# Performance work log

Hardware: AMD Instinct MI355X
Metric: run time of the kernel (lower is better)

The kernel has to match this reference:

```python
import jax, jax.numpy as jnp
from jax import lax
import numpy as np

B, H, W, D_MODEL = 2, 64, 64, 192
D_INNER, D_STATE, DT_RANK = 384, 16, 12
L = H * W
LN_EPS = 1e-5


def setup_inputs() -> dict:
    ks = jax.random.split(jax.random.key(0), 12)
    rng = np.random.default_rng(0)
    perm = rng.permutation(L).astype(np.int32)

    def p(i, shape, scale=0.02):
        return jax.random.normal(ks[i], shape, dtype=jnp.float32) * scale

    return {
        "x": jax.random.normal(ks[0], (B, H, W, D_MODEL), dtype=jnp.float32),
        "condition": jax.random.normal(ks[1], (B, H, W, D_MODEL), dtype=jnp.float32),
        "W_in": p(2, (2 * D_INNER, D_MODEL)),
        "W_con": p(3, (D_INNER, D_MODEL)),
        "conv_w": p(4, (D_INNER, 1, 3, 3)),
        "conv_b": jnp.zeros((D_INNER,), jnp.float32),
        "con_conv_w": p(5, (D_INNER, 1, 3, 3)),
        "con_conv_b": jnp.zeros((D_INNER,), jnp.float32),
        "x_proj_w": p(6, (DT_RANK + 2 * D_STATE, D_INNER)),
        "dt_proj_w": p(7, (D_INNER, DT_RANK)),
        "dt_proj_b": p(8, (D_INNER,), 0.1),
        "A_logs": jnp.tile(jnp.log(jnp.arange(1, D_STATE + 1, dtype=jnp.float32))[None, :], (D_INNER, 1)),
        "Ds": jnp.ones((D_INNER,), jnp.float32),
        "ln_w": jnp.ones((D_INNER,), jnp.float32),
        "ln_b": jnp.zeros((D_INNER,), jnp.float32),
        "W_out": p(9, (D_MODEL, D_INNER)),
        "scan_path": jnp.asarray(perm),
        "rev_scan_path": jnp.asarray(np.argsort(perm).astype(np.int32)),
    }


def _dwconv(x, w, b):
    # depthwise 3x3 conv, SAME padding; x: [B, C, H, W], w: [C, 1, 3, 3]
    y = lax.conv_general_dilated(x, w, (1, 1), "SAME",
                                 dimension_numbers=("NCHW", "OIHW", "NCHW"),
                                 feature_group_count=x.shape[1])
    return y + b[None, :, None, None]


def _selective_scan(u, delta, A, Bs, Cs, D):
    # u, delta: [B, D, L]; A: [D, N]; Bs, Cs: [B, N, L]; D: [D]
    dA = jnp.exp(jnp.einsum("bdl,dn->lbdn", delta, A))          # [L, B, D, N]
    dBu = jnp.einsum("bdl,bnl,bdl->lbdn", delta, Bs, u)          # [L, B, D, N]
    Ct = jnp.transpose(Cs, (2, 0, 1))                             # [L, B, N]
    h0 = jnp.zeros(dA.shape[1:], dA.dtype)

    def step(h, inp):
        a, b, c = inp
        h = a * h + b
        return h, jnp.einsum("bdn,bn->bd", h, c)

    _, ys = lax.scan(step, h0, (dA, dBu, Ct))                     # ys: [L, B, D]
    y = jnp.transpose(ys, (1, 2, 0))                              # [B, D, L]
    return y + u * D[None, :, None]


def _forward(x, condition, W_in, W_con, conv_w, conv_b, con_conv_w, con_conv_b,
             x_proj_w, dt_proj_w, dt_proj_b, A_logs, Ds, ln_w, ln_b, W_out,
             scan_path, rev_scan_path):
    b, h, w, _ = x.shape
    l = h * w
    xz = x @ W_in.T                                               # [B, H, W, 2*Din]
    xa, z = jnp.split(xz, 2, axis=-1)
    z = jax.nn.silu(z)
    c = condition @ W_con.T
    xa = jax.nn.silu(_dwconv(jnp.transpose(xa, (0, 3, 1, 2)), conv_w, conv_b))
    c = jax.nn.silu(_dwconv(jnp.transpose(c, (0, 3, 1, 2)), con_conv_w, con_conv_b))
    d = xa.shape[1]
    xs = xa.reshape(b, d, l)[:, :, scan_path]                     # forward_permutation, K=1
    cs = c.reshape(b, d, l)[:, :, scan_path]
    x_dbl = jnp.einsum("bdl,cd->bcl", xs + cs, x_proj_w)          # [B, R+2N, L]
    r, n = dt_proj_w.shape[1], A_logs.shape[1]
    dts = jnp.einsum("brl,dr->bdl", x_dbl[:, :r], dt_proj_w)
    Bs = x_dbl[:, r:r + n]
    Cs = x_dbl[:, r + n:]
    A = -jnp.exp(A_logs)
    delta = jax.nn.softplus(dts + dt_proj_b[None, :, None])       # delta_softplus=True
    y = _selective_scan(xs, delta, A, Bs, Cs, Ds)                 # [B, D, L]
    y = y[:, :, rev_scan_path]                                    # backward_permutation
    y = jnp.transpose(y, (0, 2, 1))                               # [B, L, D]
    mu = jnp.mean(y, axis=-1, keepdims=True)
    var = jnp.var(y, axis=-1, keepdims=True)
    y = (y - mu) * lax.rsqrt(var + LN_EPS) * ln_w + ln_b          # out_norm
    y = y.reshape(b, h, w, d) * z
    return y @ W_out.T                                            # out_proj (no bias)


def reference(x, condition, W_in, W_con, conv_w, conv_b, con_conv_w, con_conv_b,
              x_proj_w, dt_proj_w, dt_proj_b, A_logs, Ds, ln_w, ln_b, W_out,
              scan_path, rev_scan_path):
    return _forward(x, condition, W_in, W_con, conv_w, conv_b, con_conv_w,
                    con_conv_b, x_proj_w, dt_proj_w, dt_proj_b, A_logs, Ds,
                    ln_w, ln_b, W_out, scan_path, rev_scan_path)
```

## Files before the change

### kernel.cpp

```cpp
#include <hip/hip_runtime.h>
#include <math.h>

#define BB 2
#define HH 64
#define WW 64
#define DM 192
#define DI 384
#define NS 16
#define DTR 12
#define LL 4096
#define ROWS (BB*LL)
#define NCHUNK 64
#define LCHUNK 64
#define NCOMB 448

typedef __attribute__((ext_vector_type(8))) short bf16x8;
typedef __attribute__((ext_vector_type(4))) float f32x4;

__device__ __forceinline__ float silu_f(float v) {
    return v / (1.0f + __expf(-v));
}

__device__ __forceinline__ unsigned short f2bf(float f) {
    union { float f; unsigned int u; } c; c.f = f;
    unsigned int u = c.u;
    u += 0x7fffu + ((u >> 16) & 1u);
    return (unsigned short)(u >> 16);
}
__device__ __forceinline__ float bf2f(unsigned short h) {
    union { unsigned int u; float f; } c; c.u = ((unsigned int)h) << 16;
    return c.f;
}

__device__ __forceinline__ bf16x8 f2bf8(float4 a, float4 b) {
    bf16x8 r;
    r[0] = (short)f2bf(a.x); r[1] = (short)f2bf(a.y);
    r[2] = (short)f2bf(a.z); r[3] = (short)f2bf(a.w);
    r[4] = (short)f2bf(b.x); r[5] = (short)f2bf(b.y);
    r[6] = (short)f2bf(b.z); r[7] = (short)f2bf(b.w);
    return r;
}

__global__ __launch_bounds__(256) void prep_weights(
    const float* __restrict__ w_in, const float* __restrict__ w_con,
    const float* __restrict__ w_out,
    const float* __restrict__ x_proj_w, const float* __restrict__ dt_w,
    unsigned short* __restrict__ w_in_bf, unsigned short* __restrict__ w_con_bf,
    unsigned short* __restrict__ w_out_bf, unsigned short* __restrict__ wc)
{
    int idx = blockIdx.x * 256 + threadIdx.x;
    if (idx < 73728) {
        const float4* src; ushort4* dst; int off;
        if (idx < 36864)      { src = (const float4*)w_in;  dst = (ushort4*)w_in_bf;  off = idx; }
        else if (idx < 55296) { src = (const float4*)w_con; dst = (ushort4*)w_con_bf; off = idx - 36864; }
        else                  { src = (const float4*)w_out; dst = (ushort4*)w_out_bf; off = idx - 55296; }
        float4 v = src[off];
        ushort4 o;
        o.x = f2bf(v.x); o.y = f2bf(v.y); o.z = f2bf(v.z); o.w = f2bf(v.w);
        dst[off] = o;
    } else {
        int e = idx - 73728;
        if (e >= NCOMB * DI) return;
        int row = e / DI, k = e - row * DI;
        float v = 0.f;
        if (row < 384) {
            const float* dw = dt_w + row * DTR;
            #pragma unroll
            for (int r = 0; r < DTR; ++r) v += dw[r] * x_proj_w[r * DI + k];
        } else if (row < 416) {
            v = x_proj_w[(12 + (row - 384)) * DI + k];
        }
        wc[e] = f2bf(v);
    }
}

__device__ __forceinline__ void gemm_epilogue(
    int mode, int row, int col, int N, float v,
    const float* __restrict__ bias,
    float* __restrict__ out0, void* __restrict__ out1)
{
    if (mode == 0) {
        if (col < 384) out0[(size_t)row * 384 + col] = v;
        else ((unsigned short*)out1)[(size_t)row * 384 + (col - 384)] = f2bf(silu_f(v));
    } else if (mode == 1) {
        out0[(size_t)row * N + col] = v;
    } else {
        if (col < 384) {
            float a = v + bias[col];
            out0[(size_t)row * 384 + col] = (a > 20.f) ? a : log1pf(__expf(a));
        } else if (col < 416) {
            int idx = col - 384;
            int pos = (idx < 16) ? ((idx & 7) * 4 + (idx >> 3))
                                 : (((idx - 16) & 7) * 4 + 2 + ((idx - 16) >> 3));
            ((float*)out1)[(size_t)row * 32 + pos] = v;
        }
    }
}

__global__ __launch_bounds__(256) void gemm_bf16(
    const unsigned short* __restrict__ A, const unsigned short* __restrict__ W,
    const float* __restrict__ bias,
    float* __restrict__ out0, void* __restrict__ out1,
    int M, int N, int K, int mode)
{
    __shared__ __align__(16) unsigned short sA[64 * 40];
    __shared__ __align__(16) unsigned short sB[64 * 40];
    const int bm = blockIdx.x * 64;
    const int bn = blockIdx.y * 64;
    const int tid  = threadIdx.x;
    const int wave = tid >> 6;
    const int lane = tid & 63;
    const int quad = lane >> 4;
    const int l16  = lane & 15;
    const int lrow = tid >> 2;
    const int lkof = (tid & 3) * 8;

    f32x4 acc[4];
    #pragma unroll
    for (int t = 0; t < 4; ++t) acc[t] = (f32x4)(0.f);

    const int arow = (wave * 16 + l16) * 40 + quad * 8;

    for (int k0 = 0; k0 < K; k0 += 32) {
        *(bf16x8*)&sA[lrow * 40 + lkof] =
            *(const bf16x8*)&A[(size_t)(bm + lrow) * K + k0 + lkof];
        *(bf16x8*)&sB[lrow * 40 + lkof] =
            *(const bf16x8*)&W[(size_t)(bn + lrow) * K + k0 + lkof];
        __syncthreads();
        bf16x8 a = *(bf16x8*)&sA[arow];
        #pragma unroll
        for (int t = 0; t < 4; ++t) {
            bf16x8 b = *(bf16x8*)&sB[(t * 16 + l16) * 40 + quad * 8];
            acc[t] = __builtin_amdgcn_mfma_f32_16x16x32_bf16(a, b, acc[t], 0, 0, 0);
        }
        __syncthreads();
    }

    #pragma unroll
    for (int t = 0; t < 4; ++t) {
        int col = bn + t * 16 + l16;
        #pragma unroll
        for (int r = 0; r < 4; ++r) {
            int row = bm + wave * 16 + quad * 4 + r;
            gemm_epilogue(mode, row, col, N, acc[t][r], bias, out0, out1);
        }
    }
}

__global__ __launch_bounds__(256) void gemm_dual(
    const float* __restrict__ x, const float* __restrict__ cond,
    const unsigned short* __restrict__ w_in_bf,
    const unsigned short* __restrict__ w_con_bf,
    float* __restrict__ xa_pre, unsigned short* __restrict__ z_bf,
    float* __restrict__ c_pre)
{
    const int zz = blockIdx.z;
    if (zz == 1 && blockIdx.y >= 6) return;
    const float* A = zz ? cond : x;
    const unsigned short* W = zz ? w_con_bf : w_in_bf;
    float* out0 = zz ? c_pre : xa_pre;
    const int mode = zz ? 1 : 0;
    const int N = zz ? 384 : 768;

    __shared__ __align__(16) unsigned short sA[64 * 40];
    __shared__ __align__(16) unsigned short sB[64 * 40];
    const int bm = blockIdx.x * 64;
    const int bn = blockIdx.y * 64;
    const int tid  = threadIdx.x;
    const int wave = tid >> 6;
    const int lane = tid & 63;
    const int quad = lane >> 4;
    const int l16  = lane & 15;
    const int lrow = tid >> 2;
    const int lkof = (tid & 3) * 8;

    f32x4 acc[4];
    #pragma unroll
    for (int t = 0; t < 4; ++t) acc[t] = (f32x4)(0.f);

    const int arow = (wave * 16 + l16) * 40 + quad * 8;

    for (int k0 = 0; k0 < DM; k0 += 32) {
        const float* ap = &A[(size_t)(bm + lrow) * DM + k0 + lkof];
        float4 a0 = *(const float4*)ap;
        float4 a1 = *(const float4*)(ap + 4);
        *(bf16x8*)&sA[lrow * 40 + lkof] = f2bf8(a0, a1);
        *(bf16x8*)&sB[lrow * 40 + lkof] =
            *(const bf16x8*)&W[(size_t)(bn + lrow) * DM + k0 + lkof];
        __syncthreads();
        bf16x8 a = *(bf16x8*)&sA[arow];
        #pragma unroll
        for (int t = 0; t < 4; ++t) {
            bf16x8 b = *(bf16x8*)&sB[(t * 16 + l16) * 40 + quad * 8];
            acc[t] = __builtin_amdgcn_mfma_f32_16x16x32_bf16(a, b, acc[t], 0, 0, 0);
        }
        __syncthreads();
    }

    #pragma unroll
    for (int t = 0; t < 4; ++t) {
        int col = bn + t * 16 + l16;
        #pragma unroll
        for (int r = 0; r < 4; ++r) {
            int row = bm + wave * 16 + quad * 4 + r;
            gemm_epilogue(mode, row, col, N, acc[t][r], nullptr, out0, (void*)z_bf);
        }
    }
}

__global__ __launch_bounds__(256) void dwconv2_scatter(
    const float* __restrict__ xin, const float* __restrict__ cin,
    const float* __restrict__ wx, const float* __restrict__ bx,
    const float* __restrict__ wc, const float* __restrict__ bc,
    const int* __restrict__ rev_scan_path,
    float* __restrict__ xs_buf, unsigned short* __restrict__ s_bf)
{
    const int tile = blockIdx.x;
    const int c0   = blockIdx.y * 32;
    const int b    = blockIdx.z;
    const int h0 = (tile >> 3) * 8, w0 = (tile & 7) * 8;
    __shared__ float smx[10 * 10 * 32];
    __shared__ float smc[10 * 10 * 32];
    __shared__ int   jtile[64];

    for (int idx = threadIdx.x; idx < 3200; idx += 256) {
        int pix = idx >> 5, ch = idx & 31;
        int py = pix / 10, px = pix - py * 10;
        int gh = h0 + py - 1, gw = w0 + px - 1;
        float vx = 0.f, vc = 0.f;
        if (gh >= 0 && gh < 64 && gw >= 0 && gw < 64) {
            size_t g = ((size_t)(b * LL + gh * 64 + gw)) * DI + c0 + ch;
            vx = xin[g]; vc = cin[g];
        }
        smx[idx] = vx; smc[idx] = vc;
    }
    if (threadIdx.x < 64) {
        int l = (h0 + (threadIdx.x >> 3)) * 64 + (w0 + (threadIdx.x & 7));
        jtile[threadIdx.x] = rev_scan_path[l];
    }
    __syncthreads();

    const int ch = threadIdx.x & 31;
    const int pq = threadIdx.x >> 5;
    float wrx[9], wrc[9];
    #pragma unroll
    for (int k = 0; k < 9; ++k) {
        wrx[k] = wx[(c0 + ch) * 9 + k];
        wrc[k] = wc[(c0 + ch) * 9 + k];
    }
    const float bvx = bx[c0 + ch];
    const float bvc = bc[c0 + ch];

    #pragma unroll
    for (int i = 0; i < 8; ++i) {
        int p  = pq * 8 + i;
        int ph = p >> 3, pw = p & 7;
        float ax = bvx, ac = bvc;
        #pragma unroll
        for (int ki = 0; ki < 3; ++ki)
            #pragma unroll
            for (int kj = 0; kj < 3; ++kj) {
                int si = ((ph + ki) * 10 + (pw + kj)) * 32 + ch;
                ax += wrx[ki * 3 + kj] * smx[si];
                ac += wrc[ki * 3 + kj] * smc[si];
            }
        float xv = silu_f(ax);
        float sv = xv + silu_f(ac);
        size_t o = ((size_t)(b * LL + jtile[p])) * DI + c0 + ch;
        xs_buf[o] = xv;
        s_bf[o]   = f2bf(sv);
    }
}

__global__ __launch_bounds__(256) void scan_chunkA(
    const float* __restrict__ xs, const float* __restrict__ delta,
    const float* __restrict__ btct, const float* __restrict__ A_logs,
    float* __restrict__ chunkA, float* __restrict__ chunkB)
{
    const int c = blockIdx.x;
    const int g = blockIdx.y;
    const int b = blockIdx.z;
    const int t = threadIdx.x;
    const int grp = t >> 3, p = t & 7;
    const int d = g * 32 + grp;
    const float Av0 = -__expf(A_logs[d * NS + p]);
    const float Av1 = -__expf(A_logs[d * NS + p + 8]);
    const int j0 = c * LCHUNK;

    const float*  dl = delta + ((size_t)b * LL + j0) * DI + d;
    const float*  ul = xs    + ((size_t)b * LL + j0) * DI + d;
    const float2* bl = (const float2*)btct + ((size_t)b * LL + j0) * 16 + p * 2;

    float h0 = 0.f, h1 = 0.f, Sd = 0.f;
    float dv[4], uv[4]; float2 bv[4];
    #pragma unroll
    for (int q = 0; q < 4; ++q) {
        dv[q] = dl[(size_t)q * DI]; uv[q] = ul[(size_t)q * DI]; bv[q] = bl[(size_t)q * 16];
    }
    for (int j = 0; j < LCHUNK; j += 4) {
        float nd[4], nu[4]; float2 nb[4];
        if (j + 4 < LCHUNK) {
            #pragma unroll
            for (int q = 0; q < 4; ++q) {
                int jj = j + 4 + q;
                nd[q] = dl[(size_t)jj * DI]; nu[q] = ul[(size_t)jj * DI]; nb[q] = bl[(size_t)jj * 16];
            }
        }
        #pragma unroll
        for (int q = 0; q < 4; ++q) {
            float e0 = __expf(dv[q] * Av0);
            float e1 = __expf(dv[q] * Av1);
            float du = dv[q] * uv[q];
            h0 = e0 * h0 + bv[q].x * du;
            h1 = e1 * h1 + bv[q].y * du;
            Sd += dv[q];
        }
        #pragma unroll
        for (int q = 0; q < 4; ++q) { dv[q]=nd[q]; uv[q]=nu[q]; bv[q]=nb[q]; }
    }
    size_t idx = (((size_t)b * DI + d) * 8 + p) * NCHUNK + c;
    ((float2*)chunkA)[idx] = make_float2(__expf(Sd * Av0), __expf(Sd * Av1));
    ((float2*)chunkB)[idx] = make_float2(h0, h1);
}

__global__ __launch_bounds__(256) void scan_combine(
    const float* __restrict__ chunkA, const float* __restrict__ chunkB,
    float* __restrict__ hstart)
{
    const int gid = blockIdx.x * 256 + threadIdx.x;
    const float2* A2 = (const float2*)chunkA + (size_t)gid * NCHUNK;
    const float2* B2 = (const float2*)chunkB + (size_t)gid * NCHUNK;
    float2*       H2 = (float2*)hstart       + (size_t)gid * NCHUNK;
    float h0 = 0.f, h1 = 0.f;
    for (int c = 0; c < NCHUNK; ++c) {
        float2 a = A2[c], bv = B2[c];
        H2[c] = make_float2(h0, h1);
        h0 = a.x * h0 + bv.x;
        h1 = a.y * h1 + bv.y;
    }
}

__global__ __launch_bounds__(256) void scan_chunkC(
    const float* __restrict__ xs, const float* __restrict__ delta,
    const float* __restrict__ btct,
    const float* __restrict__ A_logs, const float* __restrict__ Ds,
    const float* __restrict__ hstart,
    float* __restrict__ yt)
{
    const int c = blockIdx.x;
    const int g = blockIdx.y;
    const int b = blockIdx.z;
    const int t = threadIdx.x;
    const int grp = t >> 3, p = t & 7;
    const int d = g * 32 + grp;
    const float Av0 = -__expf(A_logs[d * NS + p]);
    const float Av1 = -__expf(A_logs[d * NS + p + 8]);
    const float Dv = Ds[d];
    const int j0 = c * LCHUNK;

    const float*  dl  = delta + ((size_t)b * LL + j0) * DI + d;
    const float*  ul  = xs    + ((size_t)b * LL + j0) * DI + d;
    const float4* bcl = (const float4*)btct + ((size_t)b * LL + j0) * 8 + p;
    float* yl = yt + ((size_t)b * LL + j0) * DI + d;

    float2 h = ((const float2*)hstart)[(((size_t)b * DI + d) * 8 + p) * NCHUNK + c];
    float h0 = h.x, h1 = h.y;

    float dv[4], uv[4]; float4 bc[4];
    #pragma unroll
    for (int q = 0; q < 4; ++q) {
        dv[q] = dl[(size_t)q * DI]; uv[q] = ul[(size_t)q * DI]; bc[q] = bcl[(size_t)q * 8];
    }
    for (int j = 0; j < LCHUNK; j += 4) {
        float nd[4], nu[4]; float4 nbc[4];
        if (j + 4 < LCHUNK) {
            #pragma unroll
            for (int q = 0; q < 4; ++q) {
                int jj = j + 4 + q;
                nd[q] = dl[(size_t)jj * DI]; nu[q] = ul[(size_t)jj * DI]; nbc[q] = bcl[(size_t)jj * 8];
            }
        }
        #pragma unroll
        for (int q = 0; q < 4; ++q) {
            float e0 = __expf(dv[q] * Av0);
            float e1 = __expf(dv[q] * Av1);
            float du = dv[q] * uv[q];
            h0 = e0 * h0 + bc[q].x * du;
            h1 = e1 * h1 + bc[q].y * du;
            float acc = h0 * bc[q].z + h1 * bc[q].w;
            acc += __shfl_xor(acc, 4, 8);
            acc += __shfl_xor(acc, 2, 8);
            acc += __shfl_xor(acc, 1, 8);
            if (p == 0) yl[(size_t)(j + q) * DI] = acc + uv[q] * Dv;
        }
        #pragma unroll
        for (int q = 0; q < 4; ++q) { dv[q]=nd[q]; uv[q]=nu[q]; bc[q]=nbc[q]; }
    }
}

__global__ __launch_bounds__(128) void ln_mul(
    const float* __restrict__ yt, const unsigned short* __restrict__ z,
    const int* __restrict__ scan_path,
    const float* __restrict__ ln_w, const float* __restrict__ ln_b,
    unsigned short* __restrict__ yn)
{
    const int j = blockIdx.x;
    const int b = blockIdx.y;
    const int l = scan_path[j];
    const int t = threadIdx.x;
    const float* row = yt + ((size_t)(b * LL + j)) * DI;
    float v0 = row[t], v1 = row[t + 128], v2 = row[t + 256];
    float s  = v0 + v1 + v2;
    float s2 = v0*v0 + v1*v1 + v2*v2;
    #pragma unroll
    for (int off = 32; off > 0; off >>= 1) {
        s  += __shfl_down(s, off);
        s2 += __shfl_down(s2, off);
    }
    __shared__ float red[4];
    if ((t & 63) == 0) { red[(t >> 6) * 2] = s; red[(t >> 6) * 2 + 1] = s2; }
    __syncthreads();
    float S  = red[0] + red[2];
    float S2 = red[1] + red[3];
    float mu  = S * (1.0f / DI);
    float var = S2 * (1.0f / DI) - mu * mu;
    float inv = rsqrtf(var + 1e-5f);

    const unsigned short* zr = z + ((size_t)(b * LL + l)) * DI;
    unsigned short* o = yn + ((size_t)(b * LL + l)) * DI;
    o[t]       = f2bf(((v0 - mu) * inv * ln_w[t]       + ln_b[t])       * bf2f(zr[t]));
    o[t + 128] = f2bf(((v1 - mu) * inv * ln_w[t + 128] + ln_b[t + 128]) * bf2f(zr[t + 128]));
    o[t + 256] = f2bf(((v2 - mu) * inv * ln_w[t + 256] + ln_b[t + 256]) * bf2f(zr[t + 256]));
}

extern "C" void kernel_launch(void* const* d_in, const int* in_sizes, int n_in,
                              void* d_out, int out_size, void* d_ws, size_t ws_size,
                              hipStream_t stream) {
    const float* x          = (const float*)d_in[0];
    const float* cond       = (const float*)d_in[1];
    const float* W_in       = (const float*)d_in[2];
    const float* W_con      = (const float*)d_in[3];
    const float* conv_w     = (const float*)d_in[4];
    const float* conv_b     = (const float*)d_in[5];
    const float* con_conv_w = (const float*)d_in[6];
    const float* con_conv_b = (const float*)d_in[7];
    const float* x_proj_w   = (const float*)d_in[8];
    const float* dt_proj_w  = (const float*)d_in[9];
    const float* dt_proj_b  = (const float*)d_in[10];
    const float* A_logs     = (const float*)d_in[11];
    const float* Ds         = (const float*)d_in[12];
    const float* ln_w       = (const float*)d_in[13];
    const float* ln_b       = (const float*)d_in[14];
    const float* W_out      = (const float*)d_in[15];
    const int*   scan_path  = (const int*)d_in[16];
    const int*   rev_path   = (const int*)d_in[17];

    float* ws = (float*)d_ws;
    const size_t S  = (size_t)BB * LL * DI;
    const size_t SC = (size_t)NCHUNK * BB * DI * NS;
    float* xa_pre  = ws + 0 * S;
    float* zslab   = ws + 1 * S;
    float* c_pre   = ws + 2 * S;
    float* xs_buf  = ws + 3 * S;
    float* dl_buf  = ws + 4 * S;
    float* btct    = ws + 5 * S;
    float* chunkA  = btct + (size_t)BB * LL * 32;
    float* chunkB  = chunkA + SC;
    float* hstart  = chunkB + SC;
    float* bfpool  = hstart + SC;

    unsigned short* z_bf     = (unsigned short*)zslab;
    unsigned short* s_bf     = (unsigned short*)bfpool;
    unsigned short* w_in_bf  = s_bf + (size_t)ROWS * DI;
    unsigned short* w_con_bf = w_in_bf + 768 * DM;
    unsigned short* w_out_bf = w_con_bf + 384 * DM;
    unsigned short* wcomb_bf = w_out_bf + 192 * DI;
    unsigned short* yn_bf    = (unsigned short*)c_pre;
    float* yt = xa_pre;

    prep_weights<<<(73728 + NCOMB * DI + 255) / 256, 256, 0, stream>>>(
        W_in, W_con, W_out, x_proj_w, dt_proj_w,
        w_in_bf, w_con_bf, w_out_bf, wcomb_bf);

    gemm_dual<<<dim3(ROWS / 64, 12, 2), 256, 0, stream>>>(
        x, cond, w_in_bf, w_con_bf, xa_pre, z_bf, c_pre);
    dwconv2_scatter<<<dim3(64, 12, BB), 256, 0, stream>>>(
        xa_pre, c_pre, conv_w, conv_b, con_conv_w, con_conv_b,
        rev_path, xs_buf, s_bf);
    gemm_bf16<<<dim3(ROWS / 64, NCOMB / 64), 256, 0, stream>>>(
        s_bf, wcomb_bf, dt_proj_b, dl_buf, (void*)btct, ROWS, NCOMB, DI, 2);
    scan_chunkA<<<dim3(NCHUNK, DI / 32, BB), 256, 0, stream>>>(
        xs_buf, dl_buf, btct, A_logs, chunkA, chunkB);
    scan_combine<<<(BB * DI * 8) / 256, 256, 0, stream>>>(chunkA, chunkB, hstart);
    scan_chunkC<<<dim3(NCHUNK, DI / 32, BB), 256, 0, stream>>>(
        xs_buf, dl_buf, btct, A_logs, Ds, hstart, yt);
    ln_mul<<<dim3(LL, BB), 128, 0, stream>>>(yt, z_bf, scan_path, ln_w, ln_b, yn_bf);
    gemm_bf16<<<dim3(ROWS / 64, 192 / 64), 256, 0, stream>>>(
        yn_bf, w_out_bf, nullptr, (float*)d_out, nullptr, ROWS, DM, DI, 1);
}
```

Measured before the change: 231.8 us.

## Fuse chunked scan into single-pass kernel with decoupled lookback

Replaces the three scan kernels (chunk-local reduction, serial combine, chunk replay) with one kernel. Each block takes a dynamic ticket for its chunk, publishes its local decay and state with a release flag, then walks back over predecessor chunks with acquire spins, stopping early once the accumulated decay underflows. This removes two kernel launches and the hstart/chunk buffer round trip, at the cost of spin-waiting, serial lookback latency for later chunks and an approximation that truncates negligible contributions.

After: 454.6 us. 1.96x slower.

```diff
diff --git a/kernel.cpp b/kernel.cpp
--- a/kernel.cpp
+++ b/kernel.cpp
@@ -13,6 +13,7 @@
 #define NCHUNK 64
 #define LCHUNK 64
 #define NCOMB 448
+#define NSEQ (12*BB)
 
 typedef __attribute__((ext_vector_type(8))) short bf16x8;
 typedef __attribute__((ext_vector_type(4))) float f32x4;
@@ -46,7 +47,8 @@
     const float* __restrict__ w_out,
     const float* __restrict__ x_proj_w, const float* __restrict__ dt_w,
     unsigned short* __restrict__ w_in_bf, unsigned short* __restrict__ w_con_bf,
-    unsigned short* __restrict__ w_out_bf, unsigned short* __restrict__ wc)
+    unsigned short* __restrict__ w_out_bf, unsigned short* __restrict__ wc,
+    int* __restrict__ flags_tickets)
 {
     int idx = blockIdx.x * 256 + threadIdx.x;
     if (idx < 73728) {
@@ -58,9 +60,8 @@
         ushort4 o;
         o.x = f2bf(v.x); o.y = f2bf(v.y); o.z = f2bf(v.z); o.w = f2bf(v.w);
         dst[off] = o;
-    } else {
+    } else if (idx < 73728 + NCOMB * DI) {
         int e = idx - 73728;
-        if (e >= NCOMB * DI) return;
         int row = e / DI, k = e - row * DI;
         float v = 0.f;
         if (row < 384) {
@@ -71,6 +72,9 @@
             v = x_proj_w[(12 + (row - 384)) * DI + k];
         }
         wc[e] = f2bf(v);
+    } else {
+        int e = idx - (73728 + NCOMB * DI);
+        if (e < NSEQ * NCHUNK + NSEQ) flags_tickets[e] = 0;
     }
 }
 
@@ -272,84 +276,20 @@
     }
 }
 
-__global__ __launch_bounds__(256) void scan_chunkA(
-    const float* __restrict__ xs, const float* __restrict__ delta,
-    const float* __restrict__ btct, const float* __restrict__ A_logs,
-    float* __restrict__ chunkA, float* __restrict__ chunkB)
-{
-    const int c = blockIdx.x;
-    const int g = blockIdx.y;
-    const int b = blockIdx.z;
-    const int t = threadIdx.x;
-    const int grp = t >> 3, p = t & 7;
-    const int d = g * 32 + grp;
-    const float Av0 = -__expf(A_logs[d * NS + p]);
-    const float Av1 = -__expf(A_logs[d * NS + p + 8]);
-    const int j0 = c * LCHUNK;
-
-    const float*  dl = delta + ((size_t)b * LL + j0) * DI + d;
-    const float*  ul = xs    + ((size_t)b * LL + j0) * DI + d;
-    const float2* bl = (const float2*)btct + ((size_t)b * LL + j0) * 16 + p * 2;
-
-    float h0 = 0.f, h1 = 0.f, Sd = 0.f;
-    float dv[4], uv[4]; float2 bv[4];
-    #pragma unroll
-    for (int q = 0; q < 4; ++q) {
-        dv[q] = dl[(size_t)q * DI]; uv[q] = ul[(size_t)q * DI]; bv[q] = bl[(size_t)q * 16];
-    }
-    for (int j = 0; j < LCHUNK; j += 4) {
-        float nd[4], nu[4]; float2 nb[4];
-        if (j + 4 < LCHUNK) {
-            #pragma unroll
-            for (int q = 0; q < 4; ++q) {
-                int jj = j + 4 + q;
-                nd[q] = dl[(size_t)jj * DI]; nu[q] = ul[(size_t)jj * DI]; nb[q] = bl[(size_t)jj * 16];
-            }
-        }
-        #pragma unroll
-        for (int q = 0; q < 4; ++q) {
-            float e0 = __expf(dv[q] * Av0);
-            float e1 = __expf(dv[q] * Av1);
-            float du = dv[q] * uv[q];
-            h0 = e0 * h0 + bv[q].x * du;
-            h1 = e1 * h1 + bv[q].y * du;
-            Sd += dv[q];
-        }
-        #pragma unroll
-        for (int q = 0; q < 4; ++q) { dv[q]=nd[q]; uv[q]=nu[q]; bv[q]=nb[q]; }
-    }
-    size_t idx = (((size_t)b * DI + d) * 8 + p) * NCHUNK + c;
-    ((float2*)chunkA)[idx] = make_float2(__expf(Sd * Av0), __expf(Sd * Av1));
-    ((float2*)chunkB)[idx] = make_float2(h0, h1);
-}
-
-__global__ __launch_bounds__(256) void scan_combine(
-    const float* __restrict__ chunkA, const float* __restrict__ chunkB,
-    float* __restrict__ hstart)
-{
-    const int gid = blockIdx.x * 256 + threadIdx.x;
-    const float2* A2 = (const float2*)chunkA + (size_t)gid * NCHUNK;
-    const float2* B2 = (const float2*)chunkB + (size_t)gid * NCHUNK;
-    float2*       H2 = (float2*)hstart       + (size_t)gid * NCHUNK;
-    float h0 = 0.f, h1 = 0.f;
-    for (int c = 0; c < NCHUNK; ++c) {
-        float2 a = A2[c], bv = B2[c];
-        H2[c] = make_float2(h0, h1);
-        h0 = a.x * h0 + bv.x;
-        h1 = a.y * h1 + bv.y;
-    }
-}
-
-__global__ __launch_bounds__(256) void scan_chunkC(
+__global__ __launch_bounds__(256) void scan_single(
     const float* __restrict__ xs, const float* __restrict__ delta,
     const float* __restrict__ btct,
     const float* __restrict__ A_logs, const float* __restrict__ Ds,
-    const float* __restrict__ hstart,
-    float* __restrict__ yt)
-{
-    const int c = blockIdx.x;
+    float4* __restrict__ Loc, int* __restrict__ flags,
+    int* __restrict__ tickets, float* __restrict__ yt)
+{
     const int g = blockIdx.y;
     const int b = blockIdx.z;
+    const int seq = g * BB + b;
+    __shared__ int sc;
+    if (threadIdx.x == 0) sc = atomicAdd(&tickets[seq], 1);
+    __syncthreads();
+    const int c = sc;
     const int t = threadIdx.x;
     const int grp = t >> 3, p = t & 7;
     const int d = g * 32 + grp;
@@ -360,41 +300,96 @@
 
     const float*  dl  = delta + ((size_t)b * LL + j0) * DI + d;
     const float*  ul  = xs    + ((size_t)b * LL + j0) * DI + d;
+    const float2* bl  = (const float2*)btct + ((size_t)b * LL + j0) * 16 + p * 2;
     const float4* bcl = (const float4*)btct + ((size_t)b * LL + j0) * 8 + p;
     float* yl = yt + ((size_t)b * LL + j0) * DI + d;
 
-    float2 h = ((const float2*)hstart)[(((size_t)b * DI + d) * 8 + p) * NCHUNK + c];
-    float h0 = h.x, h1 = h.y;
-
-    float dv[4], uv[4]; float4 bc[4];
-    #pragma unroll
-    for (int q = 0; q < 4; ++q) {
-        dv[q] = dl[(size_t)q * DI]; uv[q] = ul[(size_t)q * DI]; bc[q] = bcl[(size_t)q * 8];
-    }
-    for (int j = 0; j < LCHUNK; j += 4) {
-        float nd[4], nu[4]; float4 nbc[4];
-        if (j + 4 < LCHUNK) {
+    float h0 = 0.f, h1 = 0.f, Sd = 0.f;
+    {
+        float dv[4], uv[4]; float2 bv[4];
+        #pragma unroll
+        for (int q = 0; q < 4; ++q) {
+            dv[q] = dl[(size_t)q * DI]; uv[q] = ul[(size_t)q * DI]; bv[q] = bl[(size_t)q * 16];
+        }
+        for (int j = 0; j < LCHUNK; j += 4) {
+            float nd[4], nu[4]; float2 nb[4];
+            if (j + 4 < LCHUNK) {
+                #pragma unroll
+                for (int q = 0; q < 4; ++q) {
+                    int jj = j + 4 + q;
+                    nd[q] = dl[(size_t)jj * DI]; nu[q] = ul[(size_t)jj * DI]; nb[q] = bl[(size_t)jj * 16];
+                }
+            }
             #pragma unroll
             for (int q = 0; q < 4; ++q) {
-                int jj = j + 4 + q;
-                nd[q] = dl[(size_t)jj * DI]; nu[q] = ul[(size_t)jj * DI]; nbc[q] = bcl[(size_t)jj * 8];
+                float e0 = __expf(dv[q] * Av0);
+                float e1 = __expf(dv[q] * Av1);
+                float du = dv[q] * uv[q];
+                h0 = e0 * h0 + bv[q].x * du;
+                h1 = e1 * h1 + bv[q].y * du;
+                Sd += dv[q];
             }
-        }
+            #pragma unroll
+            for (int q = 0; q < 4; ++q) { dv[q]=nd[q]; uv[q]=nu[q]; bv[q]=nb[q]; }
+        }
+    }
+    const float A0 = __expf(Sd * Av0), A1 = __expf(Sd * Av1);
+
+    const size_t lbase = ((size_t)seq * NCHUNK + c) * 256;
+    Loc[lbase + t] = make_float4(A0, A1, h0, h1);
+    __threadfence();
+    __syncthreads();
+    if (t == 0)
+        __hip_atomic_store(&flags[seq * NCHUNK + c], 1,
+                           __ATOMIC_RELEASE, __HIP_MEMORY_SCOPE_AGENT);
+
+    float hs0 = 0.f, hs1 = 0.f, P0 = 1.f, P1 = 1.f;
+    for (int i = c - 1; i >= 0; --i) {
+        if (t == 0) {
+            while (__hip_atomic_load(&flags[seq * NCHUNK + i],
+                                     __ATOMIC_ACQUIRE, __HIP_MEMORY_SCOPE_AGENT) == 0)
+                __builtin_amdgcn_s_sleep(8);
+        }
+        __syncthreads();
+        float4 L = Loc[((size_t)seq * NCHUNK + i) * 256 + t];
+        hs0 += P0 * L.z;  hs1 += P1 * L.w;
+        P0  *= L.x;       P1  *= L.y;
+        int dead = (fabsf(P0) < 1e-35f) && (fabsf(P1) < 1e-35f);
+        if (__syncthreads_and(dead)) break;
+    }
+
+    h0 = hs0; h1 = hs1;
+    {
+        float dv[4], uv[4]; float4 bc[4];
         #pragma unroll
         for (int q = 0; q < 4; ++q) {
-            float e0 = __expf(dv[q] * Av0);
-            float e1 = __expf(dv[q] * Av1);
-            float du = dv[q] * uv[q];
-            h0 = e0 * h0 + bc[q].x * du;
-            h1 = e1 * h1 + bc[q].y * du;
-            float acc = h0 * bc[q].z + h1 * bc[q].w;
-            acc += __shfl_xor(acc, 4, 8);
-            acc += __shfl_xor(acc, 2, 8);
-            acc += __shfl_xor(acc, 1, 8);
-            if (p == 0) yl[(size_t)(j + q) * DI] = acc + uv[q] * Dv;
-        }
-        #pragma unroll
-        for (int q = 0; q < 4; ++q) { dv[q]=nd[q]; uv[q]=nu[q]; bc[q]=nbc[q]; }
+            dv[q] = dl[(size_t)q * DI]; uv[q] = ul[(size_t)q * DI]; bc[q] = bcl[(size_t)q * 8];
+        }
+        for (int j = 0; j < LCHUNK; j += 4) {
+            float nd[4], nu[4]; float4 nbc[4];
+            if (j + 4 < LCHUNK) {
+                #pragma unroll
+                for (int q = 0; q < 4; ++q) {
+                    int jj = j + 4 + q;
+                    nd[q] = dl[(size_t)jj * DI]; nu[q] = ul[(size_t)jj * DI]; nbc[q] = bcl[(size_t)jj * 8];
+                }
+            }
+            #pragma unroll
+            for (int q = 0; q < 4; ++q) {
+                float e0 = __expf(dv[q] * Av0);
+                float e1 = __expf(dv[q] * Av1);
+                float du = dv[q] * uv[q];
+                h0 = e0 * h0 + bc[q].x * du;
+                h1 = e1 * h1 + bc[q].y * du;
+                float acc = h0 * bc[q].z + h1 * bc[q].w;
+                acc += __shfl_xor(acc, 4, 8);
+                acc += __shfl_xor(acc, 2, 8);
+                acc += __shfl_xor(acc, 1, 8);
+                if (p == 0) yl[(size_t)(j + q) * DI] = acc + uv[q] * Dv;
+            }
+            #pragma unroll
+            for (int q = 0; q < 4; ++q) { dv[q]=nd[q]; uv[q]=nu[q]; bc[q]=nbc[q]; }
+        }
     }
 }
 
@@ -457,17 +452,15 @@
 
     float* ws = (float*)d_ws;
     const size_t S  = (size_t)BB * LL * DI;
-    const size_t SC = (size_t)NCHUNK * BB * DI * NS;
     float* xa_pre  = ws + 0 * S;
     float* zslab   = ws + 1 * S;
     float* c_pre   = ws + 2 * S;
     float* xs_buf  = ws + 3 * S;
     float* dl_buf  = ws + 4 * S;
     float* btct    = ws + 5 * S;
-    float* chunkA  = btct + (size_t)BB * LL * 32;
-    float* chunkB  = chunkA + SC;
-    float* hstart  = chunkB + SC;
-    float* bfpool  = hstart + SC;
+    float* locbuf  = btct + (size_t)BB * LL * 32;
+    float* ftbuf   = locbuf + (size_t)NSEQ * NCHUNK * 256 * 4;
+    float* bfpool  = ftbuf + 4096;
 
     unsigned short* z_bf     = (unsigned short*)zslab;
     unsigned short* s_bf     = (unsigned short*)bfpool;
@@ -476,11 +469,13 @@
     unsigned short* w_out_bf = w_con_bf + 384 * DM;
     unsigned short* wcomb_bf = w_out_bf + 192 * DI;
     unsigned short* yn_bf    = (unsigned short*)c_pre;
+    int* flags   = (int*)ftbuf;
+    int* tickets = flags + NSEQ * NCHUNK;
     float* yt = xa_pre;
 
-    prep_weights<<<(73728 + NCOMB * DI + 255) / 256, 256, 0, stream>>>(
+    prep_weights<<<(73728 + NCOMB * DI + NSEQ * NCHUNK + NSEQ + 255) / 256, 256, 0, stream>>>(
         W_in, W_con, W_out, x_proj_w, dt_proj_w,
-        w_in_bf, w_con_bf, w_out_bf, wcomb_bf);
+        w_in_bf, w_con_bf, w_out_bf, wcomb_bf, flags);
 
     gemm_dual<<<dim3(ROWS / 64, 12, 2), 256, 0, stream>>>(
         x, cond, w_in_bf, w_con_bf, xa_pre, z_bf, c_pre);
@@ -489,11 +484,9 @@
         rev_path, xs_buf, s_bf);
     gemm_bf16<<<dim3(ROWS / 64, NCOMB / 64), 256, 0, stream>>>(
         s_bf, wcomb_bf, dt_proj_b, dl_buf, (void*)btct, ROWS, NCOMB, DI, 2);
-    scan_chunkA<<<dim3(NCHUNK, DI / 32, BB), 256, 0, stream>>>(
-        xs_buf, dl_buf, btct, A_logs, chunkA, chunkB);
-    scan_combine<<<(BB * DI * 8) / 256, 256, 0, stream>>>(chunkA, chunkB, hstart);
-    scan_chunkC<<<dim3(NCHUNK, DI / 32, BB), 256, 0, stream>>>(
-        xs_buf, dl_buf, btct, A_logs, Ds, hstart, yt);
+    scan_single<<<dim3(NCHUNK, DI / 32, BB), 256, 0, stream>>>(
+        xs_buf, dl_buf, btct, A_logs, Ds,
+        (float4*)locbuf, flags, tickets, yt);
     ln_mul<<<dim3(LL, BB), 128, 0, stream>>>(yt, z_bf, scan_path, ln_w, ln_b, yn_bf);
     gemm_bf16<<<dim3(ROWS / 64, 192 / 64), 256, 0, stream>>>(
         yn_bf, w_out_bf, nullptr, (float*)d_out, nullptr, ROWS, DM, DI, 1);
```

## Fold chunk-state combine into scan_chunkC and halve scan chunk length

Applied to the files above, without the earlier changes.

Removes the separate scan_combine kernel. Each scan_chunkC thread now rebuilds its starting state by walking backwards over earlier chunks' decay and offset values, and stops early once the accumulated decay product underflows below 1e-30. The chunk count doubles to 128 with 32 steps per chunk, which gives more parallel blocks in the chunk passes. The cost is redundant backward combine work per chunk, up to 127 steps for late chunks, and the early-exit cutoff is an approximation that relies on strong decay in the data.

New measurement: 230.0 us. Within noise of the previous version (-0.8%).

```diff
diff --git a/kernel.cpp b/kernel.cpp
--- a/kernel.cpp
+++ b/kernel.cpp
@@ -10,8 +10,8 @@
 #define DTR 12
 #define LL 4096
 #define ROWS (BB*LL)
-#define NCHUNK 64
-#define LCHUNK 64
+#define NCHUNK 128
+#define LCHUNK 32
 #define NCOMB 448
 
 typedef __attribute__((ext_vector_type(8))) short bf16x8;
@@ -323,28 +323,11 @@
     ((float2*)chunkB)[idx] = make_float2(h0, h1);
 }
 
-__global__ __launch_bounds__(256) void scan_combine(
-    const float* __restrict__ chunkA, const float* __restrict__ chunkB,
-    float* __restrict__ hstart)
-{
-    const int gid = blockIdx.x * 256 + threadIdx.x;
-    const float2* A2 = (const float2*)chunkA + (size_t)gid * NCHUNK;
-    const float2* B2 = (const float2*)chunkB + (size_t)gid * NCHUNK;
-    float2*       H2 = (float2*)hstart       + (size_t)gid * NCHUNK;
-    float h0 = 0.f, h1 = 0.f;
-    for (int c = 0; c < NCHUNK; ++c) {
-        float2 a = A2[c], bv = B2[c];
-        H2[c] = make_float2(h0, h1);
-        h0 = a.x * h0 + bv.x;
-        h1 = a.y * h1 + bv.y;
-    }
-}
-
 __global__ __launch_bounds__(256) void scan_chunkC(
     const float* __restrict__ xs, const float* __restrict__ delta,
     const float* __restrict__ btct,
     const float* __restrict__ A_logs, const float* __restrict__ Ds,
-    const float* __restrict__ hstart,
+    const float* __restrict__ chunkA, const float* __restrict__ chunkB,
     float* __restrict__ yt)
 {
     const int c = blockIdx.x;
@@ -363,8 +346,16 @@
     const float4* bcl = (const float4*)btct + ((size_t)b * LL + j0) * 8 + p;
     float* yl = yt + ((size_t)b * LL + j0) * DI + d;
 
-    float2 h = ((const float2*)hstart)[(((size_t)b * DI + d) * 8 + p) * NCHUNK + c];
-    float h0 = h.x, h1 = h.y;
+    const size_t base = (((size_t)b * DI + d) * 8 + p) * NCHUNK;
+    const float2* A2 = (const float2*)chunkA + base;
+    const float2* B2 = (const float2*)chunkB + base;
+    float h0 = 0.f, h1 = 0.f, P0 = 1.f, P1 = 1.f;
+    for (int i = c - 1; i >= 0; --i) {
+        float2 a = A2[i], bv = B2[i];
+        h0 += P0 * bv.x;  h1 += P1 * bv.y;
+        P0 *= a.x;        P1 *= a.y;
+        if (fmaxf(fabsf(P0), fabsf(P1)) < 1e-30f) break;
+    }
 
     float dv[4], uv[4]; float4 bc[4];
     #pragma unroll
@@ -466,8 +457,7 @@
     float* btct    = ws + 5 * S;
     float* chunkA  = btct + (size_t)BB * LL * 32;
     float* chunkB  = chunkA + SC;
-    float* hstart  = chunkB + SC;
-    float* bfpool  = hstart + SC;
+    float* bfpool  = chunkB + SC;
 
     unsigned short* z_bf     = (unsigned short*)zslab;
     unsigned short* s_bf     = (unsigned short*)bfpool;
@@ -491,9 +481,8 @@
         s_bf, wcomb_bf, dt_proj_b, dl_buf, (void*)btct, ROWS, NCOMB, DI, 2);
     scan_chunkA<<<dim3(NCHUNK, DI / 32, BB), 256, 0, stream>>>(
         xs_buf, dl_buf, btct, A_logs, chunkA, chunkB);
-    scan_combine<<<(BB * DI * 8) / 256, 256, 0, stream>>>(chunkA, chunkB, hstart);
     scan_chunkC<<<dim3(NCHUNK, DI / 32, BB), 256, 0, stream>>>(
-        xs_buf, dl_buf, btct, A_logs, Ds, hstart, yt);
+        xs_buf, dl_buf, btct, A_logs, Ds, chunkA, chunkB, yt);
     ln_mul<<<dim3(LL, BB), 128, 0, stream>>>(yt, z_bf, scan_path, ln_w, ln_b, yn_bf);
     gemm_bf16<<<dim3(ROWS / 64, 192 / 64), 256, 0, stream>>>(
         yn_bf, w_out_bf, nullptr, (float*)d_out, nullptr, ROWS, DM, DI, 1);
```
